# Performance work log

Hardware: AMD Instinct MI355X
Metric: run time of the kernel (lower is better)

The kernel has to match this reference:

```python
import jax, jax.numpy as jnp
import numpy as np

B, T, D = 2, 8192, 1024
H = 4
QK = D // 2          # qk_dim = hidden_size * expand_qk
V = D                # value_dim = hidden_size
HK = QK // H         # head_qk_dim = 128
HV = V // H          # head_v_dim = 256
CHUNK = 16           # GLA chunk size (small to keep exp(+-cumsum(gk)) in fp32 range)
EPS = 1e-5


def setup_inputs() -> dict:
    key = jax.random.key(0)
    ks = jax.random.split(key, 9)
    s = 0.02
    hidden_states = jax.random.normal(ks[0], (B, T, D), jnp.float32)
    Wq = jax.random.normal(ks[1], (D, QK), jnp.float32) * s
    Wk = jax.random.normal(ks[2], (D, QK), jnp.float32) * s
    Wv = jax.random.normal(ks[3], (D, V), jnp.float32) * s
    Wa = jax.random.normal(ks[4], (D, H), jnp.float32) * s
    Wg = jax.random.normal(ks[5], (D, V), jnp.float32) * s
    Wo = jax.random.normal(ks[6], (V, D), jnp.float32) * s
    # A_log / dt_bias initialized exactly as in the torch module
    A = jax.random.uniform(ks[7], (H,), jnp.float32, 0.5, 16.0)
    A_log = jnp.log(A)
    dt = jnp.exp(jax.random.uniform(ks[8], (H,), jnp.float32)
                 * (np.log(0.1) - np.log(0.001)) + np.log(0.001))
    dt = jnp.clip(dt, 1e-4, None)
    dt_bias = dt + jnp.log(-jnp.expm1(-dt))   # inverse softplus of dt
    rms_w = jnp.ones((HV,), jnp.float32)
    return {"hidden_states": hidden_states, "Wq": Wq, "Wk": Wk, "Wv": Wv,
            "Wa": Wa, "Wg": Wg, "Wo": Wo, "A_log": A_log,
            "dt_bias": dt_bias, "rms_w": rms_w}


def _gla_forward(hidden_states, Wq, Wk, Wv, Wa, Wg, Wo, A_log, dt_bias, rms_w):
    q = hidden_states @ Wq
    k = hidden_states @ Wk
    v = hidden_states @ Wv
    alpha = hidden_states @ Wa                                   # [B,T,H]
    # mamba_decay: log-space gate, negative
    gk = -jnp.exp(A_log) * jax.nn.softplus(alpha + dt_bias)      # [B,T,H]

    qh = q.reshape(B, T, H, HK)
    kh = k.reshape(B, T, H, HK)
    vh = v.reshape(B, T, H, HV)
    gkh = jnp.broadcast_to(gk[..., None], (B, T, H, HK))

    Nc = T // CHUNK

    def chunks(x):  # [B,T,H,d] -> [Nc,B,H,C,d]
        return x.reshape(B, Nc, CHUNK, H, x.shape[-1]).transpose(1, 0, 3, 2, 4)

    qc, kc, vc, gc = chunks(qh), chunks(kh), chunks(vh), chunks(gkh)
    bcum = jnp.cumsum(gc, axis=-2)            # inclusive cumulative log-decay
    scale = HK ** -0.5                        # default scale in chunk_gla

    q_g = qc * jnp.exp(bcum) * scale          # [Nc,B,H,C,K]
    # intra-chunk causal scores: A_ij = q_i . (k_j * exp(b_i - b_j)), j <= i
    Ascore = jnp.einsum('nbhik,nbhjk->nbhij', q_g, kc * jnp.exp(-bcum))
    mask = jnp.tril(jnp.ones((CHUNK, CHUNK), bool))
    Ascore = jnp.where(mask, Ascore, 0.0)
    o_intra = jnp.einsum('nbhij,nbhjv->nbhiv', Ascore, vc)

    b_last = bcum[..., -1:, :]                # [Nc,B,H,1,K]
    k_out = kc * jnp.exp(b_last - bcum)       # keys decayed to chunk end

    def step(S, inp):
        qg, ko, vv, bl = inp                  # per-chunk slices
        o_inter = jnp.einsum('bhck,bhkv->bhcv', qg, S)
        S = jnp.exp(bl[..., 0, :])[..., None] * S \
            + jnp.einsum('bhck,bhcv->bhkv', ko, vv)
        return S, o_inter

    S0 = jnp.zeros((B, H, HK, HV), jnp.float32)
    _, o_inter = jax.lax.scan(step, S0, (q_g, k_out, vc, b_last))

    o = (o_intra + o_inter).transpose(1, 0, 3, 2, 4).reshape(B, T, H, HV)

    # fused per-head RMSNorm + swish output gate
    g = (hidden_states @ Wg).reshape(B, T, H, HV)
    o_n = o * jax.lax.rsqrt(jnp.mean(o * o, axis=-1, keepdims=True) + EPS) * rms_w
    o = o_n * (g * jax.nn.sigmoid(g))
    return o.reshape(B, T, V) @ Wo


def reference(hidden_states, Wq, Wk, Wv, Wa, Wg, Wo, A_log, dt_bias, rms_w):
    return _gla_forward(hidden_states, Wq, Wk, Wv, Wa, Wg, Wo,
                        A_log, dt_bias, rms_w)
```

## Files before the change

### kernel.cpp

```cpp
#include <hip/hip_runtime.h>
#include <cstdint>
#include <cstddef>

#define NB 2
#define NT 8192
#define ND 1024
#define NH 4
#define NV 1024
#define NHK 128
#define NHV 256
#define CHK 64
#define NCHK 128
#define QKS 1024
#define SCALE 0.08838834764831845f

using f32x4 = __attribute__((ext_vector_type(4))) float;
using short8 = __attribute__((ext_vector_type(8))) short;
using s16x4 = __attribute__((ext_vector_type(4))) short;

__device__ __forceinline__ float bf2f(unsigned short u){
  union { unsigned int i; float f; } t; t.i = ((unsigned int)u) << 16; return t.f;
}
__device__ __forceinline__ unsigned short f2bf(float f){
  union { float f; unsigned int i; } t; t.f = f;
  unsigned int r = t.i + 0x7fffu + ((t.i >> 16) & 1u);
  return (unsigned short)(r >> 16);
}
__device__ __forceinline__ double shfl_up_dbl(double v, int off){
  union { double d; unsigned int u[2]; } a, r;
  a.d = v;
  r.u[0] = __shfl_up(a.u[0], off, 64);
  r.u[1] = __shfl_up(a.u[1], off, 64);
  return r.d;
}
__device__ __forceinline__ void* lds_at(void* base, int row, int colElem, int rowBytes){
  return (void*)((char*)base + row*rowBytes + (((colElem*2) ^ ((row&7)<<4))));
}
__device__ __forceinline__ int osw(int rowl, int byteoff){
  return rowl*512 + (byteoff ^ (((rowl>>2)&7)<<4));
}

typedef const __attribute__((address_space(1))) unsigned int as1_u32;
typedef __attribute__((address_space(3))) unsigned int as3_u32;
__device__ __forceinline__ void gl_lds16(const void* g_lane, void* lds_uniform){
  __builtin_amdgcn_global_load_lds((as1_u32*)(uintptr_t)g_lane,
                                   (as3_u32*)(unsigned int)(uintptr_t)lds_uniform,
                                   16, 0, 0);
}

__global__ __launch_bounds__(256) void k_tc(const float* __restrict__ src,
                                            unsigned short* __restrict__ dst, int R, int C){
  int idx = blockIdx.x*256 + threadIdx.x;
  if (idx >= R*C) return;
  int r = idx % R, c = idx / R;
  dst[(size_t)c*R + r] = f2bf(src[(size_t)r*C + c]);
}

__global__ __launch_bounds__(256) void k_tc2(const float* __restrict__ src,
                                             unsigned short* __restrict__ dh,
                                             unsigned short* __restrict__ dl, int R, int C){
  int idx = blockIdx.x*256 + threadIdx.x;
  if (idx >= R*C) return;
  int r = idx % R, c = idx / R;
  float x = src[(size_t)r*C + c];
  unsigned short h = f2bf(x);
  unsigned short l = f2bf(x - bf2f(h));
  dh[(size_t)c*R + r] = h;
  dl[(size_t)c*R + r] = l;
}

__global__ __launch_bounds__(256) void k_alphacast(const float* __restrict__ hs,
                                                   const float* __restrict__ Wa,
                                                   const float* __restrict__ Al,
                                                   const float* __restrict__ dtb,
                                                   float* __restrict__ Gc,
                                                   unsigned short* __restrict__ hsh){
  int rowi = blockIdx.x;
  int tid = threadIdx.x;
  const float* h = hs + (size_t)rowi*ND;
  f32x4 x = *(const f32x4*)(h + tid*4);
  s16x4 hb;
  #pragma unroll
  for (int e=0;e<4;e++) hb[e] = (short)f2bf(x[e]);
  *(s16x4*)(hsh + (size_t)rowi*ND + tid*4) = hb;
  float a0=0.f,a1=0.f,a2=0.f,a3=0.f;
  #pragma unroll
  for (int e=0;e<4;e++){
    int d = tid*4+e;
    a0 += x[e]*Wa[d*4+0]; a1 += x[e]*Wa[d*4+1]; a2 += x[e]*Wa[d*4+2]; a3 += x[e]*Wa[d*4+3];
  }
  #pragma unroll
  for (int off=32; off>0; off>>=1){
    a0 += __shfl_down(a0, off, 64); a1 += __shfl_down(a1, off, 64);
    a2 += __shfl_down(a2, off, 64); a3 += __shfl_down(a3, off, 64);
  }
  __shared__ float red[4][4];
  if ((tid&63)==0){ int w = tid>>6; red[w][0]=a0; red[w][1]=a1; red[w][2]=a2; red[w][3]=a3; }
  __syncthreads();
  if (tid < 4){
    float al = red[0][tid]+red[1][tid]+red[2][tid]+red[3][tid];
    float xx = al + dtb[tid];
    float sp = (xx > 20.f) ? xx : log1pf(expf(xx));
    float gkv = -expf(Al[tid]) * sp;
    int bb = rowi >> 13, t = rowi & (NT-1);
    Gc[((size_t)(bb*NH + tid))*NT + t] = gkv;
  }
}

template<int BSPLIT, int GSWISH>
__global__ __launch_bounds__(256, BSPLIT ? 3 : 4)
void k_gemm2(const unsigned short* __restrict__ A2h,
             const unsigned short* __restrict__ Bth,
             const unsigned short* __restrict__ Btl,
             unsigned short* __restrict__ C, int M, int N, int K){
  __shared__ unsigned short sA[2][4096];
  __shared__ unsigned short sB[2][4096];
  __shared__ unsigned short sBl[BSPLIT ? 2*4096 : 8];
  int tid = threadIdx.x, lane = tid & 63, wave = tid >> 6;
  int m0 = blockIdx.x*128, n0 = blockIdx.y*128;
  int wr = (wave>>1)*64, wc = (wave&1)*64;
  int row = lane & 15, kq = (lane>>4)*8;
  int rS = lane>>2, cS = (lane&3)*8;
  f32x4 acc[4][4];
  #pragma unroll
  for (int m=0;m<4;m++)
    #pragma unroll
    for (int n=0;n<4;n++)
      #pragma unroll
      for (int r=0;r<4;r++) acc[m][n][r] = 0.f;

  auto STAGE = [&](int buf, int k0){
    #pragma unroll
    for (int half=0; half<2; ++half){
      int rb = half*64 + wave*16;
      size_t gArow = (size_t)(m0 + rb + rS)*K + k0 + cS;
      size_t gBrow = (size_t)(n0 + rb + rS)*K + k0 + cS;
      gl_lds16(A2h + gArow, &sA[buf][rb*32]);
      gl_lds16(Bth + gBrow, &sB[buf][rb*32]);
      if (BSPLIT) gl_lds16(Btl + gBrow, &sBl[buf*4096 + rb*32]);
    }
  };

  STAGE(0, 0);
  __syncthreads();
  int nsteps = K >> 5;
  for (int t=0; t<nsteps; ++t){
    int cur = t & 1;
    if (t+1 < nsteps) STAGE(cur^1, (t+1)*32);
    short8 ah[4], bh[4];
    #pragma unroll
    for (int m=0;m<4;m++) ah[m] = *(const short8*)(&sA[cur][(wr + m*16 + row)*32 + kq]);
    #pragma unroll
    for (int n=0;n<4;n++) bh[n] = *(const short8*)(&sB[cur][(wc + n*16 + row)*32 + kq]);
    #pragma unroll
    for (int m=0;m<4;m++)
      #pragma unroll
      for (int n=0;n<4;n++)
        acc[m][n] = __builtin_amdgcn_mfma_f32_16x16x32_bf16(ah[m], bh[n], acc[m][n], 0, 0, 0);
    if (BSPLIT){
      short8 bl[4];
      #pragma unroll
      for (int n=0;n<4;n++) bl[n] = *(const short8*)(&sBl[cur*4096 + (wc + n*16 + row)*32 + kq]);
      #pragma unroll
      for (int m=0;m<4;m++)
        #pragma unroll
        for (int n=0;n<4;n++)
          acc[m][n] = __builtin_amdgcn_mfma_f32_16x16x32_bf16(ah[m], bl[n], acc[m][n], 0, 0, 0);
    }
    __syncthreads();
  }
  #pragma unroll
  for (int m=0;m<4;m++)
    #pragma unroll
    for (int n=0;n<4;n++)
      #pragma unroll
      for (int r=0;r<4;r++){
        int rr = m0 + wr + m*16 + (lane>>4)*4 + r;
        int cc = n0 + wc + n*16 + (lane&15);
        float v = acc[m][n][r];
        if (GSWISH) v = v / (1.f + expf(-v));
        C[(size_t)rr*N + cc] = f2bf(v);
      }
}

__global__ __launch_bounds__(256, 4) void k_gemm(const unsigned short* __restrict__ A,
                                                 const unsigned short* __restrict__ Bt,
                                                 float* __restrict__ C, int M, int N, int K){
  __shared__ unsigned short sA[2][4096];
  __shared__ unsigned short sB[2][4096];
  int tid = threadIdx.x, lane = tid & 63, wave = tid >> 6;
  int m0 = blockIdx.x*128, n0 = blockIdx.y*128;
  int wr = (wave>>1)*64, wc = (wave&1)*64;
  int row = lane & 15, kq = (lane>>4)*8;
  int rS = lane>>2, cS = (lane&3)*8;
  f32x4 acc[4][4];
  #pragma unroll
  for (int m=0;m<4;m++)
    #pragma unroll
    for (int n=0;n<4;n++)
      #pragma unroll
      for (int r=0;r<4;r++) acc[m][n][r] = 0.f;

  auto STAGE = [&](int buf, int k0){
    #pragma unroll
    for (int half=0; half<2; ++half){
      int rb = half*64 + wave*16;
      size_t gArow = (size_t)(m0 + rb + rS)*K + k0 + cS;
      size_t gBrow = (size_t)(n0 + rb + rS)*K + k0 + cS;
      gl_lds16(A  + gArow, &sA[buf][rb*32]);
      gl_lds16(Bt + gBrow, &sB[buf][rb*32]);
    }
  };

  STAGE(0, 0);
  __syncthreads();
  int nsteps = K >> 5;
  for (int t=0; t<nsteps; ++t){
    int cur = t & 1;
    if (t+1 < nsteps) STAGE(cur^1, (t+1)*32);
    short8 af[4], bfr[4];
    #pragma unroll
    for (int m=0;m<4;m++) af[m]  = *(const short8*)(&sA[cur][(wr + m*16 + row)*32 + kq]);
    #pragma unroll
    for (int n=0;n<4;n++) bfr[n] = *(const short8*)(&sB[cur][(wc + n*16 + row)*32 + kq]);
    #pragma unroll
    for (int m=0;m<4;m++)
      #pragma unroll
      for (int n=0;n<4;n++)
        acc[m][n] = __builtin_amdgcn_mfma_f32_16x16x32_bf16(af[m], bfr[n], acc[m][n], 0, 0, 0);
    __syncthreads();
  }
  #pragma unroll
  for (int m=0;m<4;m++)
    #pragma unroll
    for (int n=0;n<4;n++)
      #pragma unroll
      for (int r=0;r<4;r++){
        int rr = m0 + wr + m*16 + (lane>>4)*4 + r;
        int cc = n0 + wc + n*16 + (lane&15);
        C[(size_t)rr*N + cc] = acc[m][n][r];
      }
}

__global__ __launch_bounds__(256) void k_cumsum(const float* __restrict__ Gc, double* __restrict__ Gd){
  int bh = blockIdx.x, tid = threadIdx.x;
  const float* g = Gc + (size_t)bh*NT;
  double* out = Gd + (size_t)bh*NT;
  __shared__ double wsum[4];
  __shared__ double carry_s;
  if (tid==0) carry_s = 0.0;
  __syncthreads();
  for (int t0=0; t0<NT; t0+=256){
    double v = (double)g[t0+tid];
    #pragma unroll
    for (int off=1; off<64; off<<=1){
      double y = shfl_up_dbl(v, off);
      if ((tid&63) >= off) v += y;
    }
    if ((tid&63)==63) wsum[tid>>6] = v;
    __syncthreads();
    double add = carry_s;
    for (int w=0; w<(tid>>6); ++w) add += wsum[w];
    v += add;
    out[t0+tid] = v;
    __syncthreads();
    if (tid==255) carry_s = v;
    __syncthreads();
  }
}

__global__ __launch_bounds__(256, 2) void k_phaseA(const unsigned short* __restrict__ qkb,
                                                   const unsigned short* __restrict__ vb,
                                                   const double* __restrict__ Gd,
                                                   unsigned short* __restrict__ Sbc){
  __shared__ unsigned short vT[16384];
  __shared__ unsigned short wkT[8192];
  int blk = blockIdx.x, bh = blockIdx.y;
  int bb = bh>>2, hh = bh&3;
  int cs = blk*CHK, tid = threadIdx.x;
  int lane = tid & 63, w = tid >> 6;
  const double* Gb = Gd + (size_t)bh*NT;
  double Gend = Gb[cs + 63];
  #pragma unroll
  for (int it=0; it<8; ++it){
    int task = it*256 + tid;
    int j = task & 63, ng = task >> 6;
    short8 vv = *(const short8*)(vb + (size_t)(bb*NT + cs + j)*NV + hh*NHV + ng*8);
    #pragma unroll
    for (int e=0;e<8;e++)
      *(unsigned short*)lds_at(vT, ng*8+e, j, 128) = (unsigned short)vv[e];
  }
  #pragma unroll
  for (int it=0; it<4; ++it){
    int task = it*256 + tid;
    int j = task & 63, kg = task >> 6;
    float wj = expf((float)(Gend - Gb[cs + j]));
    short8 kv = *(const short8*)(qkb + (size_t)(bb*NT + cs + j)*QKS + 512 + hh*NHK + kg*8);
    #pragma unroll
    for (int e=0;e<8;e++)
      *(unsigned short*)lds_at(wkT, kg*8+e, j, 128) = f2bf(wj * bf2f((unsigned short)kv[e]));
  }
  __syncthreads();
  f32x4 sa[32];
  #pragma unroll
  for (int i=0;i<32;i++) sa[i] = (f32x4){0.f,0.f,0.f,0.f};
  short8 wa[2][2];
  #pragma unroll
  for (int mt=0;mt<2;mt++)
    #pragma unroll
    for (int kk=0;kk<2;kk++)
      wa[mt][kk] = *(short8*)lds_at(wkT, 32*w + mt*16 + (lane&15), kk*32 + (lane>>4)*8, 128);
  #pragma unroll
  for (int mt=0;mt<2;mt++)
    #pragma unroll
    for (int nt=0;nt<16;nt++)
      #pragma unroll
      for (int kk=0;kk<2;kk++){
        short8 b = *(short8*)lds_at(vT, nt*16 + (lane&15), kk*32 + (lane>>4)*8, 128);
        sa[mt*16+nt] = __builtin_amdgcn_mfma_f32_16x16x32_bf16(wa[mt][kk], b, sa[mt*16+nt], 0,0,0);
      }
  unsigned short* dst = Sbc + (size_t)(bh*NCHK + blk)*32768;
  #pragma unroll
  for (int mt=0;mt<2;mt++)
    #pragma unroll
    for (int nt=0;nt<16;nt++){
      int k = 32*w + mt*16 + (lane>>4)*4;
      int n = nt*16 + (lane&15);
      s16x4 p;
      #pragma unroll
      for (int r=0;r<4;r++) p[r] = (short)f2bf(sa[mt*16+nt][r]);
      *(s16x4*)(dst + (size_t)n*128 + k) = p;
    }
}

__global__ __launch_bounds__(256) void k_phaseB(unsigned short* __restrict__ Sbc,
                                                const double* __restrict__ Gd){
  int slice = blockIdx.x, bh = blockIdx.y;
  int tid = threadIdx.x;
  const double* Gb = Gd + (size_t)bh*NT;
  unsigned short* base = Sbc + (size_t)(bh*NCHK)*32768 + slice*1024 + tid*4;
  s16x4 c0 = *(const s16x4*)(base);
  f32x4 run;
  #pragma unroll
  for (int e=0;e<4;e++) run[e] = bf2f((unsigned short)c0[e]);
  s16x4 n0 = *(const s16x4*)(base + (size_t)1*32768);
  s16x4 n1 = *(const s16x4*)(base + (size_t)2*32768);
  s16x4 n2 = *(const s16x4*)(base + (size_t)3*32768);
  s16x4 n3 = *(const s16x4*)(base + (size_t)4*32768);
#define PB_STEP(U, BB) \
  { float resc = expf((float)(Gb[(BB)*CHK + 63] - Gb[(BB)*CHK - 1])); \
    s16x4 o_; \
    _Pragma("unroll") \
    for (int e=0;e<4;e++){ run[e] = resc*run[e] + bf2f((unsigned short)U[e]); o_[e] = (short)f2bf(run[e]); } \
    *(s16x4*)(base + (size_t)(BB)*32768) = o_; }
  for (int b=1; b<NCHK; b+=4){
    s16x4 u0=n0, u1=n1, u2=n2, u3=n3;
    if (b+4 < NCHK) n0 = *(const s16x4*)(base + (size_t)(b+4)*32768);
    if (b+5 < NCHK) n1 = *(const s16x4*)(base + (size_t)(b+5)*32768);
    if (b+6 < NCHK) n2 = *(const s16x4*)(base + (size_t)(b+6)*32768);
    if (b+7 < NCHK) n3 = *(const s16x4*)(base + (size_t)(b+7)*32768);
    PB_STEP(u0, b)
    if (b+1 < NCHK) PB_STEP(u1, b+1)
    if (b+2 < NCHK) PB_STEP(u2, b+2)
    if (b+3 < NCHK) PB_STEP(u3, b+3)
  }
#undef PB_STEP
}

__global__ __launch_bounds__(256, 3) void k_phaseC(const unsigned short* __restrict__ qkb,
                                                   const unsigned short* __restrict__ vb,
                                                   unsigned short* __restrict__ gio,
                                                   const float* __restrict__ rmsw,
                                                   const double* __restrict__ Gd,
                                                   const unsigned short* __restrict__ Sbc){
  __shared__ unsigned short vT[16384];
  __shared__ unsigned short scp[4096];
  __shared__ float Gsf[64];
  __shared__ float sI[64];
  __shared__ float rsum[64][4];
  __shared__ float frl[64];
  __shared__ float rms_s[256];
  int blk = blockIdx.x, bh = blockIdx.y;
  int bb = bh>>2, hh = bh&3;
  int cs = blk*CHK, tid = threadIdx.x;
  int lane = tid&63, w = tid>>6;
  const double* Gb = Gd + (size_t)bh*NT;
  rms_s[tid] = rmsw[tid];
  if (tid < 64){
    double ref = (cs == 0) ? 0.0 : Gb[cs-1];
    float g = (float)(Gb[cs+tid] - ref);
    Gsf[tid] = g;
    sI[tid] = SCALE * expf(g);
  }
  #pragma unroll
  for (int it=0; it<8; ++it){
    int task = it*256 + tid;
    int j = task & 63, ng = task >> 6;
    short8 vv = *(const short8*)(vb + (size_t)(bb*NT + cs + j)*NV + hh*NHV + ng*8);
    #pragma unroll
    for (int e=0;e<8;e++)
      *(unsigned short*)lds_at(vT, ng*8+e, j, 128) = (unsigned short)vv[e];
  }
  f32x4 oa[16];
  #pragma unroll
  for (int i=0;i<16;i++) oa[i] = (f32x4){0.f,0.f,0.f,0.f};
  if (blk > 0){
    const unsigned short* Sst = Sbc + (size_t)(bh*NCHK + blk - 1)*32768;
    #pragma unroll
    for (int kk=0;kk<4;kk++){
      short8 qrg[4];
      #pragma unroll
      for (int rg=0;rg<4;rg++)
        qrg[rg] = *(const short8*)(qkb + (size_t)(bb*NT + cs + rg*16 + (lane&15))*QKS
                                   + hh*NHK + kk*32 + (lane>>4)*8);
      #pragma unroll
      for (int nt=0;nt<4;nt++){
        short8 b = *(const short8*)(Sst + (size_t)(w*64 + nt*16 + (lane&15))*128
                                    + kk*32 + (lane>>4)*8);
        #pragma unroll
        for (int rg=0;rg<4;rg++)
          oa[rg*4+nt] = __builtin_amdgcn_mfma_f32_16x16x32_bf16(qrg[rg], b, oa[rg*4+nt], 0,0,0);
      }
    }
  }
  __syncthreads();
  if (blk > 0){
    #pragma unroll
    for (int rg=0;rg<4;rg++)
      #pragma unroll
      for (int r=0;r<4;r++){
        float srow = sI[rg*16 + (lane>>4)*4 + r];
        #pragma unroll
        for (int nt=0;nt<4;nt++) oa[rg*4+nt][r] *= srow;
      }
  }
  f32x4 pa[4];
  #pragma unroll
  for (int jt=0;jt<4;jt++) pa[jt] = (f32x4){0.f,0.f,0.f,0.f};
  {
    short8 qown[4];
    #pragma unroll
    for (int kk=0;kk<4;kk++)
      qown[kk] = *(const short8*)(qkb + (size_t)(bb*NT + cs + 16*w + (lane&15))*QKS
                                  + hh*NHK + kk*32 + (lane>>4)*8);
    #pragma unroll
    for (int jt=0;jt<4;jt++)
      #pragma unroll
      for (int kk=0;kk<4;kk++){
        short8 b = *(const short8*)(qkb + (size_t)(bb*NT + cs + jt*16 + (lane&15))*QKS
                                    + 512 + hh*NHK + kk*32 + (lane>>4)*8);
        pa[jt] = __builtin_amdgcn_mfma_f32_16x16x32_bf16(qown[kk], b, pa[jt], 0,0,0);
      }
  }
  #pragma unroll
  for (int jt=0;jt<4;jt++)
    #pragma unroll
    for (int r=0;r<4;r++){
      int il = 16*w + (lane>>4)*4 + r;
      int jl = jt*16 + (lane&15);
      float wgt = (jl <= il) ? SCALE * expf(Gsf[il] - Gsf[jl]) : 0.f;
      *(unsigned short*)lds_at(scp, il, jl, 128) = f2bf(wgt * pa[jt][r]);
    }
  __syncthreads();
  short8 af[4][2];
  #pragma unroll
  for (int rg=0;rg<4;rg++)
    #pragma unroll
    for (int kk=0;kk<2;kk++)
      af[rg][kk] = *(short8*)lds_at(scp, rg*16 + (lane&15), kk*32 + (lane>>4)*8, 128);
  #pragma unroll
  for (int nt=0;nt<4;nt++){
    short8 b0 = *(short8*)lds_at(vT, w*64 + nt*16 + (lane&15), 0*32 + (lane>>4)*8, 128);
    short8 b1 = *(short8*)lds_at(vT, w*64 + nt*16 + (lane&15), 1*32 + (lane>>4)*8, 128);
    #pragma unroll
    for (int rg=0;rg<4;rg++){
      oa[rg*4+nt] = __builtin_amdgcn_mfma_f32_16x16x32_bf16(af[rg][0], b0, oa[rg*4+nt], 0,0,0);
      oa[rg*4+nt] = __builtin_amdgcn_mfma_f32_16x16x32_bf16(af[rg][1], b1, oa[rg*4+nt], 0,0,0);
    }
  }
  float pp[16];
  #pragma unroll
  for (int rg=0;rg<4;rg++)
    #pragma unroll
    for (int r=0;r<4;r++){
      float s = 0.f;
      #pragma unroll
      for (int nt=0;nt<4;nt++) s += oa[rg*4+nt][r]*oa[rg*4+nt][r];
      pp[rg*4+r] = s;
    }
  #pragma unroll
  for (int i=0;i<16;i++){
    #pragma unroll
    for (int off=1; off<16; off<<=1) pp[i] += __shfl_xor(pp[i], off, 16);
  }
  if ((lane&15) == 0){
    int l4 = lane>>4;
    #pragma unroll
    for (int rg=0;rg<4;rg++)
      #pragma unroll
      for (int r=0;r<4;r++)
        rsum[rg*16 + l4*4 + r][w] = pp[rg*4+r];
  }
  __syncthreads();
  if (tid < 64)
    frl[tid] = rsqrtf((rsum[tid][0]+rsum[tid][1]+rsum[tid][2]+rsum[tid][3])*(1.f/256.f) + 1e-5f);
  __syncthreads();
  char* oLDS = (char*)vT;
  float fv[4][4];
  #pragma unroll
  for (int rg=0;rg<4;rg++)
    #pragma unroll
    for (int r=0;r<4;r++) fv[rg][r] = frl[rg*16 + (lane>>4)*4 + r];
  #pragma unroll
  for (int nt=0;nt<4;nt++){
    int n = w*64 + nt*16 + (lane&15);
    float rw = rms_s[n];
    #pragma unroll
    for (int rg=0;rg<4;rg++)
      #pragma unroll
      for (int r=0;r<4;r++){
        int rowl = rg*16 + (lane>>4)*4 + r;
        *(unsigned short*)(oLDS + osw(rowl, n*2)) = f2bf(oa[rg*4+nt][r] * fv[rg][r] * rw);
      }
  }
  __syncthreads();
  #pragma unroll
  for (int it=0; it<8; ++it){
    int task = it*256 + tid;
    int rowl = task >> 5, c8 = (task & 31)*8;
    size_t gbase = (size_t)(bb*NT + cs + rowl)*NV + hh*NHV + c8;
    short8 g8 = *(const short8*)(gio + gbase);
    short8 o8 = *(const short8*)(oLDS + osw(rowl, c8*2));
    short8 out;
    #pragma unroll
    for (int e=0;e<8;e++)
      out[e] = (short)f2bf(bf2f((unsigned short)o8[e]) * bf2f((unsigned short)g8[e]));
    *(short8*)(gio + gbase) = out;
  }
}

extern "C" void kernel_launch(void* const* d_in, const int* in_sizes, int n_in,
                              void* d_out, int out_size, void* d_ws, size_t ws_size,
                              hipStream_t stream) {
  (void)in_sizes; (void)n_in; (void)out_size;
  const float* hs  = (const float*)d_in[0];
  const float* Wq  = (const float*)d_in[1];
  const float* Wk  = (const float*)d_in[2];
  const float* Wv  = (const float*)d_in[3];
  const float* Wa  = (const float*)d_in[4];
  const float* Wg  = (const float*)d_in[5];
  const float* Wo  = (const float*)d_in[6];
  const float* Al  = (const float*)d_in[7];
  const float* dtb = (const float*)d_in[8];
  const float* rmsw= (const float*)d_in[9];
  char* ws = (char*)d_ws;

  constexpr size_t MB = 1048576;
  constexpr size_t OFF_QK   = 0;
  constexpr size_t OFF_V    = 32*MB;
  constexpr size_t OFF_G    = 64*MB;
  constexpr size_t OFF_WQKH = 96*MB;
  constexpr size_t OFF_WQKL = 98*MB;
  constexpr size_t OFF_WV   = 100*MB;
  constexpr size_t OFF_WG   = 102*MB;
  constexpr size_t OFF_WO   = 104*MB;
  constexpr size_t OFF_GC   = 106*MB;
  constexpr size_t OFF_GD   = 106*MB + 262144;
  constexpr size_t OFF_SBC  = 107*MB;
  constexpr size_t WS_REQUIRED = 176947200;
  if (ws_size < WS_REQUIRED) return;

  unsigned short* qkb  = (unsigned short*)(ws + OFF_QK);
  unsigned short* vb   = (unsigned short*)(ws + OFF_V);
  unsigned short* gb   = (unsigned short*)(ws + OFF_G);
  unsigned short* wqkh = (unsigned short*)(ws + OFF_WQKH);
  unsigned short* wqkl = (unsigned short*)(ws + OFF_WQKL);
  unsigned short* wvt  = (unsigned short*)(ws + OFF_WV);
  unsigned short* wgt  = (unsigned short*)(ws + OFF_WG);
  unsigned short* wot  = (unsigned short*)(ws + OFF_WO);
  float* Gc   = (float*)(ws + OFF_GC);
  double* Gd  = (double*)(ws + OFF_GD);
  unsigned short* Sbc = (unsigned short*)(ws + OFF_SBC);
  unsigned short* hsh = (unsigned short*)(ws + OFF_SBC);

  k_alphacast<<<16384, 256, 0, stream>>>(hs, Wa, Al, dtb, Gc, hsh);
  k_tc2<<<2048, 256, 0, stream>>>(Wq, wqkh, wqkl, 1024, 512);
  k_tc2<<<2048, 256, 0, stream>>>(Wk, wqkh + 512*1024, wqkl + 512*1024, 1024, 512);
  k_tc<<<4096, 256, 0, stream>>>(Wv, wvt, 1024, 1024);
  k_tc<<<4096, 256, 0, stream>>>(Wg, wgt, 1024, 1024);
  k_tc<<<4096, 256, 0, stream>>>(Wo, wot, 1024, 1024);

  k_gemm2<1,0><<<dim3(128,8), 256, 0, stream>>>(hsh, wqkh, wqkl, qkb, 16384, 1024, 1024);
  k_gemm2<0,0><<<dim3(128,8), 256, 0, stream>>>(hsh, wvt, nullptr, vb, 16384, 1024, 1024);
  k_gemm2<0,1><<<dim3(128,8), 256, 0, stream>>>(hsh, wgt, nullptr, gb, 16384, 1024, 1024);

  k_cumsum<<<8, 256, 0, stream>>>(Gc, Gd);

  k_phaseA<<<dim3(NCHK,8), 256, 0, stream>>>(qkb, vb, Gd, Sbc);
  k_phaseB<<<dim3(32,8), 256, 0, stream>>>(Sbc, Gd);
  k_phaseC<<<dim3(NCHK,8), 256, 0, stream>>>(qkb, vb, gb, rmsw, Gd, Sbc);

  k_gemm<<<dim3(128,8), 256, 0, stream>>>(gb, wot, (float*)d_out, 16384, 1024, 1024);
}
```

Baseline: 432.7 us.

## Merge V and G projections into one GEMM, fuse weight casts, add XCD swizzle

Concatenates the Wv and Wg transposed weights so the V and gate projections run as a single 16384x2048 GEMM. The swish is applied only to the gate half, and the output is an interleaved [V|G] buffer with row stride 2048 that phaseA, phaseC and the output GEMM read through a new lda argument. The five weight transpose/cast launches become one kernel. An XCD-aware block-index swizzle is added to both GEMM kernels to improve L2 locality. This cuts launch count and overhead, at the cost of strided row access into the wider combined buffer.

```diff
diff --git a/kernel.cpp b/kernel.cpp
--- a/kernel.cpp
+++ b/kernel.cpp
@@ -7,11 +7,12 @@
 #define ND 1024
 #define NH 4
 #define NV 1024
+#define NHV 256
 #define NHK 128
-#define NHV 256
 #define CHK 64
 #define NCHK 128
 #define QKS 1024
+#define VGS 2048
 #define SCALE 0.08838834764831845f
 
 using f32x4 = __attribute__((ext_vector_type(4))) float;
@@ -39,6 +40,13 @@
 __device__ __forceinline__ int osw(int rowl, int byteoff){
   return rowl*512 + (byteoff ^ (((rowl>>2)&7)<<4));
 }
+__device__ __forceinline__ void xcd_swizzle(int gx, int gy, int& bx, int& by){
+  int flat = blockIdx.y*gx + blockIdx.x;
+  int total = gx*gy;
+  int wg = (flat & 7)*(total >> 3) + (flat >> 3);
+  bx = wg / gy;
+  by = wg % gy;
+}
 
 typedef const __attribute__((address_space(1))) unsigned int as1_u32;
 typedef __attribute__((address_space(3))) unsigned int as3_u32;
@@ -48,25 +56,36 @@
                                    16, 0, 0);
 }
 
-__global__ __launch_bounds__(256) void k_tc(const float* __restrict__ src,
-                                            unsigned short* __restrict__ dst, int R, int C){
-  int idx = blockIdx.x*256 + threadIdx.x;
-  if (idx >= R*C) return;
-  int r = idx % R, c = idx / R;
-  dst[(size_t)c*R + r] = f2bf(src[(size_t)r*C + c]);
-}
-
-__global__ __launch_bounds__(256) void k_tc2(const float* __restrict__ src,
-                                             unsigned short* __restrict__ dh,
-                                             unsigned short* __restrict__ dl, int R, int C){
-  int idx = blockIdx.x*256 + threadIdx.x;
-  if (idx >= R*C) return;
-  int r = idx % R, c = idx / R;
-  float x = src[(size_t)r*C + c];
-  unsigned short h = f2bf(x);
-  unsigned short l = f2bf(x - bf2f(h));
-  dh[(size_t)c*R + r] = h;
-  dl[(size_t)c*R + r] = l;
+__global__ __launch_bounds__(256) void k_tcall(const float* __restrict__ Wq,
+                                               const float* __restrict__ Wk,
+                                               const float* __restrict__ Wv,
+                                               const float* __restrict__ Wg,
+                                               const float* __restrict__ Wo,
+                                               unsigned short* __restrict__ wqkh,
+                                               unsigned short* __restrict__ wqkl,
+                                               unsigned short* __restrict__ wvgt,
+                                               unsigned short* __restrict__ wot){
+  int b = blockIdx.x, tid = threadIdx.x;
+  if (b < 4096){
+    const float* src = (b < 2048) ? Wq : Wk;
+    int boff = (b < 2048) ? 0 : 512*1024;
+    int idx = (b & 2047)*256 + tid;
+    int r = idx & 1023, c = idx >> 10;
+    float x = src[(size_t)r*512 + c];
+    unsigned short h = f2bf(x);
+    wqkh[boff + c*1024 + r] = h;
+    wqkl[boff + c*1024 + r] = f2bf(x - bf2f(h));
+  } else if (b < 12288){
+    const float* src = (b < 8192) ? Wv : Wg;
+    int boff = (b < 8192) ? 0 : 1024*1024;
+    int idx = ((b - 4096) & 4095)*256 + tid;
+    int r = idx & 1023, c = idx >> 10;
+    wvgt[boff + c*1024 + r] = f2bf(src[(size_t)r*1024 + c]);
+  } else {
+    int idx = (b - 12288)*256 + tid;
+    int r = idx & 1023, c = idx >> 10;
+    wot[c*1024 + r] = f2bf(Wo[(size_t)r*1024 + c]);
+  }
 }
 
 __global__ __launch_bounds__(256) void k_alphacast(const float* __restrict__ hs,
@@ -117,7 +136,9 @@
   __shared__ unsigned short sB[2][4096];
   __shared__ unsigned short sBl[BSPLIT ? 2*4096 : 8];
   int tid = threadIdx.x, lane = tid & 63, wave = tid >> 6;
-  int m0 = blockIdx.x*128, n0 = blockIdx.y*128;
+  int bx, by;
+  xcd_swizzle(gridDim.x, gridDim.y, bx, by);
+  int m0 = bx*128, n0 = by*128;
   int wr = (wave>>1)*64, wc = (wave&1)*64;
   int row = lane & 15, kq = (lane>>4)*8;
   int rS = lane>>2, cS = (lane&3)*8;
@@ -169,6 +190,7 @@
     }
     __syncthreads();
   }
+  bool dosw = (GSWISH == 2) && (n0 >= 1024);
   #pragma unroll
   for (int m=0;m<4;m++)
     #pragma unroll
@@ -178,18 +200,21 @@
         int rr = m0 + wr + m*16 + (lane>>4)*4 + r;
         int cc = n0 + wc + n*16 + (lane&15);
         float v = acc[m][n][r];
-        if (GSWISH) v = v / (1.f + expf(-v));
+        if (dosw) v = v / (1.f + expf(-v));
         C[(size_t)rr*N + cc] = f2bf(v);
       }
 }
 
 __global__ __launch_bounds__(256, 4) void k_gemm(const unsigned short* __restrict__ A,
                                                  const unsigned short* __restrict__ Bt,
-                                                 float* __restrict__ C, int M, int N, int K){
+                                                 float* __restrict__ C, int M, int N, int K,
+                                                 int lda){
   __shared__ unsigned short sA[2][4096];
   __shared__ unsigned short sB[2][4096];
   int tid = threadIdx.x, lane = tid & 63, wave = tid >> 6;
-  int m0 = blockIdx.x*128, n0 = blockIdx.y*128;
+  int bx, by;
+  xcd_swizzle(gridDim.x, gridDim.y, bx, by);
+  int m0 = bx*128, n0 = by*128;
   int wr = (wave>>1)*64, wc = (wave&1)*64;
   int row = lane & 15, kq = (lane>>4)*8;
   int rS = lane>>2, cS = (lane&3)*8;
@@ -205,7 +230,7 @@
     #pragma unroll
     for (int half=0; half<2; ++half){
       int rb = half*64 + wave*16;
-      size_t gArow = (size_t)(m0 + rb + rS)*K + k0 + cS;
+      size_t gArow = (size_t)(m0 + rb + rS)*lda + k0 + cS;
       size_t gBrow = (size_t)(n0 + rb + rS)*K + k0 + cS;
       gl_lds16(A  + gArow, &sA[buf][rb*32]);
       gl_lds16(Bt + gBrow, &sB[buf][rb*32]);
@@ -270,7 +295,7 @@
 }
 
 __global__ __launch_bounds__(256, 2) void k_phaseA(const unsigned short* __restrict__ qkb,
-                                                   const unsigned short* __restrict__ vb,
+                                                   const unsigned short* __restrict__ vgb,
                                                    const double* __restrict__ Gd,
                                                    unsigned short* __restrict__ Sbc){
   __shared__ unsigned short vT[16384];
@@ -285,7 +310,7 @@
   for (int it=0; it<8; ++it){
     int task = it*256 + tid;
     int j = task & 63, ng = task >> 6;
-    short8 vv = *(const short8*)(vb + (size_t)(bb*NT + cs + j)*NV + hh*NHV + ng*8);
+    short8 vv = *(const short8*)(vgb + (size_t)(bb*NT + cs + j)*VGS + hh*NHV + ng*8);
     #pragma unroll
     for (int e=0;e<8;e++)
       *(unsigned short*)lds_at(vT, ng*8+e, j, 128) = (unsigned short)vv[e];
@@ -368,8 +393,7 @@
 }
 
 __global__ __launch_bounds__(256, 3) void k_phaseC(const unsigned short* __restrict__ qkb,
-                                                   const unsigned short* __restrict__ vb,
-                                                   unsigned short* __restrict__ gio,
+                                                   unsigned short* __restrict__ vgb,
                                                    const float* __restrict__ rmsw,
                                                    const double* __restrict__ Gd,
                                                    const unsigned short* __restrict__ Sbc){
@@ -396,7 +420,7 @@
   for (int it=0; it<8; ++it){
     int task = it*256 + tid;
     int j = task & 63, ng = task >> 6;
-    short8 vv = *(const short8*)(vb + (size_t)(bb*NT + cs + j)*NV + hh*NHV + ng*8);
+    short8 vv = *(const short8*)(vgb + (size_t)(bb*NT + cs + j)*VGS + hh*NHV + ng*8);
     #pragma unroll
     for (int e=0;e<8;e++)
       *(unsigned short*)lds_at(vT, ng*8+e, j, 128) = (unsigned short)vv[e];
@@ -528,14 +552,14 @@
   for (int it=0; it<8; ++it){
     int task = it*256 + tid;
     int rowl = task >> 5, c8 = (task & 31)*8;
-    size_t gbase = (size_t)(bb*NT + cs + rowl)*NV + hh*NHV + c8;
-    short8 g8 = *(const short8*)(gio + gbase);
+    size_t gbase = (size_t)(bb*NT + cs + rowl)*VGS + 1024 + hh*NHV + c8;
+    short8 g8 = *(const short8*)(vgb + gbase);
     short8 o8 = *(const short8*)(oLDS + osw(rowl, c8*2));
     short8 out;
     #pragma unroll
     for (int e=0;e<8;e++)
       out[e] = (short)f2bf(bf2f((unsigned short)o8[e]) * bf2f((unsigned short)g8[e]));
-    *(short8*)(gio + gbase) = out;
+    *(short8*)(vgb + gbase) = out;
   }
 }
 
@@ -557,12 +581,10 @@
 
   constexpr size_t MB = 1048576;
   constexpr size_t OFF_QK   = 0;
-  constexpr size_t OFF_V    = 32*MB;
-  constexpr size_t OFF_G    = 64*MB;
+  constexpr size_t OFF_VG   = 32*MB;
   constexpr size_t OFF_WQKH = 96*MB;
   constexpr size_t OFF_WQKL = 98*MB;
-  constexpr size_t OFF_WV   = 100*MB;
-  constexpr size_t OFF_WG   = 102*MB;
+  constexpr size_t OFF_WVG  = 100*MB;
   constexpr size_t OFF_WO   = 104*MB;
   constexpr size_t OFF_GC   = 106*MB;
   constexpr size_t OFF_GD   = 106*MB + 262144;
@@ -571,12 +593,10 @@
   if (ws_size < WS_REQUIRED) return;
 
   unsigned short* qkb  = (unsigned short*)(ws + OFF_QK);
-  unsigned short* vb   = (unsigned short*)(ws + OFF_V);
-  unsigned short* gb   = (unsigned short*)(ws + OFF_G);
+  unsigned short* vgb  = (unsigned short*)(ws + OFF_VG);
   unsigned short* wqkh = (unsigned short*)(ws + OFF_WQKH);
   unsigned short* wqkl = (unsigned short*)(ws + OFF_WQKL);
-  unsigned short* wvt  = (unsigned short*)(ws + OFF_WV);
-  unsigned short* wgt  = (unsigned short*)(ws + OFF_WG);
+  unsigned short* wvgt = (unsigned short*)(ws + OFF_WVG);
   unsigned short* wot  = (unsigned short*)(ws + OFF_WO);
   float* Gc   = (float*)(ws + OFF_GC);
   double* Gd  = (double*)(ws + OFF_GD);
@@ -584,21 +604,16 @@
   unsigned short* hsh = (unsigned short*)(ws + OFF_SBC);
 
   k_alphacast<<<16384, 256, 0, stream>>>(hs, Wa, Al, dtb, Gc, hsh);
-  k_tc2<<<2048, 256, 0, stream>>>(Wq, wqkh, wqkl, 1024, 512);
-  k_tc2<<<2048, 256, 0, stream>>>(Wk, wqkh + 512*1024, wqkl + 512*1024, 1024, 512);
-  k_tc<<<4096, 256, 0, stream>>>(Wv, wvt, 1024, 1024);
-  k_tc<<<4096, 256, 0, stream>>>(Wg, wgt, 1024, 1024);
-  k_tc<<<4096, 256, 0, stream>>>(Wo, wot, 1024, 1024);
+  k_tcall<<<16384, 256, 0, stream>>>(Wq, Wk, Wv, Wg, Wo, wqkh, wqkl, wvgt, wot);
 
   k_gemm2<1,0><<<dim3(128,8), 256, 0, stream>>>(hsh, wqkh, wqkl, qkb, 16384, 1024, 1024);
-  k_gemm2<0,0><<<dim3(128,8), 256, 0, stream>>>(hsh, wvt, nullptr, vb, 16384, 1024, 1024);
-  k_gemm2<0,1><<<dim3(128,8), 256, 0, stream>>>(hsh, wgt, nullptr, gb, 16384, 1024, 1024);
+  k_gemm2<0,2><<<dim3(128,16), 256, 0, stream>>>(hsh, wvgt, nullptr, vgb, 16384, 2048, 1024);
 
   k_cumsum<<<8, 256, 0, stream>>>(Gc, Gd);
 
-  k_phaseA<<<dim3(NCHK,8), 256, 0, stream>>>(qkb, vb, Gd, Sbc);
+  k_phaseA<<<dim3(NCHK,8), 256, 0, stream>>>(qkb, vgb, Gd, Sbc);
   k_phaseB<<<dim3(32,8), 256, 0, stream>>>(Sbc, Gd);
-  k_phaseC<<<dim3(NCHK,8), 256, 0, stream>>>(qkb, vb, gb, rmsw, Gd, Sbc);
-
-  k_gemm<<<dim3(128,8), 256, 0, stream>>>(gb, wot, (float*)d_out, 16384, 1024, 1024);
-}
+  k_phaseC<<<dim3(NCHK,8), 256, 0, stream>>>(qkb, vgb, rmsw, Gd, Sbc);
+
+  k_gemm<<<dim3(128,8), 256, 0, stream>>>(vgb + 1024, wot, (float*)d_out, 16384, 1024, 1024, VGS);
+}
```

Result: faster. 420.4 us (median of 2 runs) (-2.9%).
